# Kernel optimization log

Hardware: AMD Instinct MI355X
Metric: run time of the kernel (lower is better)

## Reference

```python
import jax, jax.numpy as jnp
import numpy as np
import math

N, S, D, BF, K, NT, NL = 4096, 64, 256, 24, 8, 64, 4096

def setup_inputs() -> dict:
    key = jax.random.key(0)
    ks = jax.random.split(key, 20)
    inp = {
        "values": jax.random.normal(ks[0], (N, S), dtype=jnp.float32),
        "kinds": jax.random.randint(ks[1], (N, S), 0, K, dtype=jnp.int32),
        "mask": jax.random.randint(ks[2], (N, S), 0, 2, dtype=jnp.int32),
        "prim_type": jax.random.randint(ks[3], (N,), 0, NT, dtype=jnp.int32),
        "layer_id": jax.random.randint(ks[4], (N,), 0, NL, dtype=jnp.int32),
        "meta": jax.random.normal(ks[5], (N, 4), dtype=jnp.float32),
        # frozen Fourier projection (sigma=8)
        "B_ff": jax.random.normal(ks[6], (1, BF), dtype=jnp.float32) * 8.0,
        # embeddings (N(0,1) like nn.Embedding default)
        "kind_emb_w": jax.random.normal(ks[7], (K, D), dtype=jnp.float32),
        "type_emb_w": jax.random.normal(ks[8], (NT, D), dtype=jnp.float32),
        "layer_emb_w": jax.random.normal(ks[9], (NL, D), dtype=jnp.float32),
        # per-kind MLPs: 2B -> D -> D
        "mlp_w1": jax.random.normal(ks[10], (K, 2 * BF, D), dtype=jnp.float32) / np.sqrt(2 * BF),
        "mlp_b1": jnp.zeros((K, D), dtype=jnp.float32),
        "mlp_w2": jax.random.normal(ks[11], (K, D, D), dtype=jnp.float32) / np.sqrt(D),
        "mlp_b2": jnp.zeros((K, D), dtype=jnp.float32),
        # fuse: 3D -> D -> D
        "fuse_w1": jax.random.normal(ks[12], (3 * D, D), dtype=jnp.float32) / np.sqrt(3 * D),
        "fuse_b1": jnp.zeros((D,), dtype=jnp.float32),
        "fuse_w2": jax.random.normal(ks[13], (D, D), dtype=jnp.float32) / np.sqrt(D),
        "fuse_b2": jnp.zeros((D,), dtype=jnp.float32),
        # meta_lin: 4 -> D
        "meta_w": jax.random.normal(ks[14], (4, D), dtype=jnp.float32) / 2.0,
        "meta_b": jnp.zeros((D,), dtype=jnp.float32),
    }
    return inp

def _gelu(x):
    return jax.nn.gelu(x, approximate=False)  # torch nn.GELU default = exact erf

def reference(values, kinds, mask, prim_type, layer_id, meta, B_ff,
              kind_emb_w, type_emb_w, layer_emb_w,
              mlp_w1, mlp_b1, mlp_w2, mlp_b2,
              fuse_w1, fuse_b1, fuse_w2, fuse_b2, meta_w, meta_b):
    n, s = values.shape
    d = kind_emb_w.shape[1]
    k_kinds = kind_emb_w.shape[0]
    # Fourier features over all N*S scalar slots -> [NS, 2B]
    y = (2.0 * math.pi) * values.reshape(-1, 1) @ B_ff
    ff = jnp.concatenate([jnp.sin(y), jnp.cos(y)], axis=-1)
    kf = kinds.reshape(-1)
    # kind-routed per-kind MLP (dispatch/combine expressed as masked combine)
    out = jnp.zeros((n * s, d), dtype=values.dtype)
    for k in range(k_kinds):
        h = _gelu(ff @ mlp_w1[k] + mlp_b1[k]) @ mlp_w2[k] + mlp_b2[k]
        out = jnp.where((kf == k)[:, None], h, out)
    h_slots = out.reshape(n, s, d) + kind_emb_w[kinds]
    m = mask.astype(values.dtype)
    h_slots = h_slots * m[..., None]
    denom = jnp.clip(m.sum(axis=1, keepdims=True), 1.0)  # [N,1]
    h_num = h_slots.sum(axis=1) / denom  # masked mean pooling -> [N,D]
    h = jnp.concatenate([h_num, type_emb_w[prim_type], layer_emb_w[layer_id]], axis=-1)
    fused = _gelu(h @ fuse_w1 + fuse_b1) @ fuse_w2 + fuse_b2
    return fused + meta @ meta_w + meta_b
```

## Files before the change

kernel.cpp:

```cpp
#include <hip/hip_runtime.h>
#include <math.h>


#define W2F_HI   0
#define W2F_LO   524288
#define W1F_HI   1048576
#define W1F_LO   1179648
#define FW1F_HI  1310720
#define FW1F_LO  1507328
#define FW2F_HI  1703936
#define FW2F_LO  1769472

#define PSTR 260

typedef __attribute__((ext_vector_type(8))) short frag;
typedef __attribute__((ext_vector_type(4))) float f32x4;

__device__ __forceinline__ unsigned short f2bf_rn(float x) {
    unsigned int u = __float_as_uint(x);
    unsigned int r = (u + 0x7fffu + ((u >> 16) & 1u)) >> 16;
    return (unsigned short)r;
}
__device__ __forceinline__ float bf2f(unsigned short h) {
    return __uint_as_float(((unsigned int)h) << 16);
}
__device__ __forceinline__ void split_bf(float x, unsigned short& h, unsigned short& l) {
    unsigned short hh = f2bf_rn(x);
    h = hh;
    l = f2bf_rn(x - bf2f(hh));
}

__device__ __forceinline__ float gelu_fast(float x) {
    float u = fabsf(x) * 0.7071067811865476f;
    float t = __builtin_amdgcn_rcpf(fmaf(0.3275911f, u, 1.0f));
    float p = fmaf(fmaf(fmaf(fmaf(1.061405429f, t, -1.453152027f), t,
                             1.421413741f), t, -0.284496736f), t, 0.254829592f) * t;
    float e = __expf(-u * u);
    float er = fmaf(-p, e, 1.0f);
    er = copysignf(er, x);
    return 0.5f * x * (1.0f + er);
}

__global__ __launch_bounds__(512) void prep_kernel(
    const float* __restrict__ w1, const float* __restrict__ w2,
    const float* __restrict__ fw1, const float* __restrict__ fw2,
    short* __restrict__ ws)
{
    int tid = blockIdx.x * 512 + threadIdx.x;
    int fid = tid >> 6, ln = tid & 63;
    if (fid >= 1792) return;
    int lr = ln & 15, kq = ln >> 4;
    float v[8];
    int dhi, dlo, dsto;
    if (fid < 1024) {
        int k = fid >> 7, kst = (fid >> 4) & 7, nt = fid & 15;
        int col = nt * 16 + lr;
        #pragma unroll
        for (int b = 0; b < 8; ++b) {
            int kg = kst * 32 + kq * 8 + b;
            v[b] = w2[(k * 256 + kg) * 256 + col];
        }
        dsto = fid * 512 + ln * 8; dhi = W2F_HI; dlo = W2F_LO;
    } else if (fid < 1280) {
        int f = fid - 1024;
        int k = f >> 5, kst = (f >> 4) & 1, nt = f & 15;
        int col = nt * 16 + lr;
        #pragma unroll
        for (int b = 0; b < 8; ++b) {
            int kg = kst * 32 + kq * 8 + b;
            v[b] = (kg < 48) ? w1[(k * 48 + kg) * 256 + col] : 0.0f;
        }
        dsto = f * 512 + ln * 8; dhi = W1F_HI; dlo = W1F_LO;
    } else if (fid < 1664) {
        int f = fid - 1280;
        int kst = f >> 4, nt = f & 15;
        int col = nt * 16 + lr;
        #pragma unroll
        for (int b = 0; b < 8; ++b) {
            int kg = kst * 32 + kq * 8 + b;
            v[b] = fw1[kg * 256 + col];
        }
        dsto = f * 512 + ln * 8; dhi = FW1F_HI; dlo = FW1F_LO;
    } else {
        int f = fid - 1664;
        int kst = f >> 4, nt = f & 15;
        int col = nt * 16 + lr;
        #pragma unroll
        for (int b = 0; b < 8; ++b) {
            int kg = kst * 32 + kq * 8 + b;
            v[b] = fw2[kg * 256 + col];
        }
        dsto = f * 512 + ln * 8; dhi = FW2F_HI; dlo = FW2F_LO;
    }
    union { unsigned short u[8]; frag f; } hu, lu;
    #pragma unroll
    for (int b = 0; b < 8; ++b) split_bf(v[b], hu.u[b], lu.u[b]);
    *(frag*)(ws + dhi + dsto) = hu.f;
    *(frag*)(ws + dlo + dsto) = lu.f;
}

__global__ __launch_bounds__(512, 1) void mono_kernel(
    const float* __restrict__ values, const int* __restrict__ kinds,
    const int* __restrict__ mask, const float* __restrict__ B_ff,
    const float* __restrict__ b1, const short* __restrict__ wsf,
    const int* __restrict__ pt, const int* __restrict__ lid,
    const float* __restrict__ meta, const float* __restrict__ type_emb,
    const float* __restrict__ layer_emb, const float* __restrict__ b2,
    const float* __restrict__ kind_emb, const float* __restrict__ fb1,
    const float* __restrict__ fb2, const float* __restrict__ meta_w,
    const float* __restrict__ meta_b, float* __restrict__ out)
{
    __shared__ __align__(16) float pool_ls[8 * 16 * PSTR];
    __shared__ float vals_ls[1024];
    __shared__ unsigned char knd_ls[1024], msk_ls[1024];
    __shared__ unsigned short list[1152];
    __shared__ short chunk_kind[80], chunk_base[80];
    __shared__ int totk_ls[8];
    __shared__ float b1_ls[2048];
    __shared__ float Bs_ls[24];
    __shared__ float cnt_ls[128], den_ls[16], meta_ls[64];
    __shared__ int pt_ls[16], lid_ls[16];

    const int t = threadIdx.x, blk = blockIdx.x;
    const int wv = t >> 6, ln = t & 63, lr16 = ln & 15, kq = ln >> 4;
    const int gbase = blk * 1024, rb = blk * 16;

    const short* w1f_hi  = wsf + W1F_HI;
    const short* w1f_lo  = wsf + W1F_LO;
    const short* w2f_hi  = wsf + W2F_HI;
    const short* w2f_lo  = wsf + W2F_LO;
    const short* fw1f_hi = wsf + FW1F_HI;
    const short* fw1f_lo = wsf + FW1F_LO;
    const short* fw2f_hi = wsf + FW2F_HI;
    const short* fw2f_lo = wsf + FW2F_LO;

    #pragma unroll
    for (int i = 0; i < 2; ++i) {
        int p = t + i * 512;
        vals_ls[p] = values[gbase + p];
        knd_ls[p]  = (unsigned char)kinds[gbase + p];
        msk_ls[p]  = (unsigned char)mask[gbase + p];
    }
    #pragma unroll
    for (int i = 0; i < 4; ++i) b1_ls[t + i * 512] = b1[t + i * 512];
    if (t < 24) Bs_ls[t] = B_ff[t];
    if (t >= 32 && t < 48) { pt_ls[t - 32] = pt[rb + t - 32]; lid_ls[t - 32] = lid[rb + t - 32]; }
    if (t >= 64 && t < 128) meta_ls[t - 64] = meta[rb * 4 + (t - 64)];
    for (int i = t; i < 8 * 16 * PSTR; i += 512) pool_ls[i] = 0.0f;
    __syncthreads();

    {
        const int k = wv;
        int tot = 0;
        #pragma unroll 1
        for (int c = 0; c < 16; ++c) {
            int p = c * 64 + ln;
            int kd = knd_ls[p], mk = msk_ls[p];
            unsigned long long bal = __ballot(mk && (kd == k));
            int pc = __popcll(bal);
            if (ln == 0) cnt_ls[c * 8 + k] = (float)pc;
            tot += pc;
            if (k == 0) {
                unsigned long long balm = __ballot(mk != 0);
                if (ln == 0) {
                    int tm = __popcll(balm);
                    den_ls[c] = 1.0f / (float)(tm > 0 ? tm : 1);
                }
            }
        }
        if (ln == 0) totk_ls[k] = tot;
    }
    __syncthreads();

    int offe = 0, cbase = 0, nch = 0;
    #pragma unroll
    for (int j = 0; j < 8; ++j) {
        int pj = (totk_ls[j] + 15) & ~15;
        if (j < wv) { offe += pj; cbase += pj >> 4; }
        nch += pj >> 4;
    }

    {
        const int k = wv;
        const unsigned long long below = (1ull << ln) - 1ull;
        int fill = 0;
        #pragma unroll 1
        for (int c = 0; c < 16; ++c) {
            int p = c * 64 + ln;
            int kd = knd_ls[p], mk = msk_ls[p];
            unsigned long long bal = __ballot(mk && (kd == k));
            if (mk && (kd == k)) list[offe + fill + __popcll(bal & below)] = (unsigned short)p;
            fill += __popcll(bal);
        }
        int padded = (fill + 15) & ~15;
        for (int i = fill + ln; i < padded; i += 64) list[offe + i] = 0xFFFFu;
        int nk = padded >> 4;
        for (int j = ln; j < nk; j += 64) {
            chunk_kind[cbase + j] = (short)k;
            chunk_base[cbase + j] = (short)(offe + j * 16);
        }
    }
    __syncthreads();

    for (int m = wv; m < nch; m += 8) {
        const int k = (int)chunk_kind[m];
        const int cb = (int)chunk_base[m];
        int slot = list[cb + lr16];
        float v = vals_ls[slot & 1023];
        v = (slot == 0xFFFF) ? 0.0f : v;

        frag ah[2], al[2];
        #pragma unroll
        for (int kst = 0; kst < 2; ++kst) {
            union { unsigned short u[8]; frag f; } hu, lu;
            int jb0 = kst * 32 + kq * 8;
            #pragma unroll
            for (int b = 0; b < 8; ++b) {
                int jb = jb0 + b;
                float sv;
                if (jb < 48) {
                    int jm = (jb < 24) ? jb : jb - 24;
                    float cadd = (jb < 24) ? 0.0f : 0.25f;
                    float rev = __builtin_amdgcn_fractf(fmaf(v, Bs_ls[jm], cadd));
                    sv = __builtin_amdgcn_sinf(rev);
                } else {
                    sv = 0.0f;
                }
                split_bf(sv, hu.u[b], lu.u[b]);
            }
            ah[kst] = hu.f; al[kst] = lu.f;
        }

        int e4[4];
        #pragma unroll
        for (int r = 0; r < 4; ++r) {
            int sl = list[cb + kq * 4 + r];
            e4[r] = (sl == 0xFFFF) ? -1 : ((sl >> 6) & 15);
        }

        #pragma unroll 4
        for (int nt = 0; nt < 16; ++nt) {
            int o0 = ((k * 2 + 0) * 16 + nt) * 512 + ln * 8;
            int o1 = ((k * 2 + 1) * 16 + nt) * 512 + ln * 8;
            frag bh0 = *(const frag*)(w1f_hi + o0);
            frag bl0 = *(const frag*)(w1f_lo + o0);
            frag bh1 = *(const frag*)(w1f_hi + o1);
            frag bl1 = *(const frag*)(w1f_lo + o1);
            f32x4 acc = (f32x4)0.0f;
            acc = __builtin_amdgcn_mfma_f32_16x16x32_bf16(ah[0], bh0, acc, 0, 0, 0);
            acc = __builtin_amdgcn_mfma_f32_16x16x32_bf16(al[0], bh0, acc, 0, 0, 0);
            acc = __builtin_amdgcn_mfma_f32_16x16x32_bf16(ah[0], bl0, acc, 0, 0, 0);
            acc = __builtin_amdgcn_mfma_f32_16x16x32_bf16(ah[1], bh1, acc, 0, 0, 0);
            acc = __builtin_amdgcn_mfma_f32_16x16x32_bf16(al[1], bh1, acc, 0, 0, 0);
            acc = __builtin_amdgcn_mfma_f32_16x16x32_bf16(ah[1], bl1, acc, 0, 0, 0);
            float b1v = b1_ls[k * 256 + nt * 16 + lr16];
            #pragma unroll
            for (int r = 0; r < 4; ++r) {
                if (e4[r] >= 0) {
                    float g = gelu_fast(acc[r] + b1v);
                    atomicAdd(&pool_ls[(k * 16 + e4[r]) * PSTR + nt * 16 + lr16], g);
                }
            }
        }
    }
    __syncthreads();

    f32x4 acc[2];
    acc[0] = (f32x4)0.0f; acc[1] = (f32x4)0.0f;

    for (int k = 0; k < 8; ++k) {
        #pragma unroll 2
        for (int kst = 0; kst < 8; ++kst) {
            const float* pp = &pool_ls[(k * 16 + lr16) * PSTR + kst * 32 + kq * 8];
            f32x4 u0 = *(const f32x4*)pp;
            f32x4 u1 = *(const f32x4*)(pp + 4);
            union { unsigned short u[8]; frag f; } hu, lu;
            #pragma unroll
            for (int b = 0; b < 4; ++b) {
                split_bf(u0[b], hu.u[b], lu.u[b]);
                split_bf(u1[b], hu.u[b + 4], lu.u[b + 4]);
            }
            frag ah = hu.f, al = lu.f;
            #pragma unroll
            for (int n = 0; n < 2; ++n) {
                int bo = ((k * 8 + kst) * 16 + (wv * 2 + n)) * 512 + ln * 8;
                frag bh = *(const frag*)(w2f_hi + bo);
                frag bl = *(const frag*)(w2f_lo + bo);
                acc[n] = __builtin_amdgcn_mfma_f32_16x16x32_bf16(ah, bh, acc[n], 0, 0, 0);
                acc[n] = __builtin_amdgcn_mfma_f32_16x16x32_bf16(al, bh, acc[n], 0, 0, 0);
                acc[n] = __builtin_amdgcn_mfma_f32_16x16x32_bf16(ah, bl, acc[n], 0, 0, 0);
            }
        }
    }
    __syncthreads();

    float* hz = pool_ls;

    #pragma unroll
    for (int n = 0; n < 2; ++n) {
        int col = (wv * 2 + n) * 16 + lr16;
        float bks[8];
        #pragma unroll
        for (int k = 0; k < 8; ++k) bks[k] = b2[k * 256 + col] + kind_emb[k * 256 + col];
        #pragma unroll
        for (int r = 0; r < 4; ++r) {
            int row = kq * 4 + r;
            float hv = acc[n][r];
            #pragma unroll
            for (int k = 0; k < 8; ++k) hv = fmaf(cnt_ls[row * 8 + k], bks[k], hv);
            hv *= den_ls[row];
            hz[row * 256 + ((((col >> 2) ^ (row & 7)) << 2) | (col & 3))] = hv;
        }
    }
    __syncthreads();

    f32x4 az[2];
    az[0] = (f32x4)0.0f; az[1] = (f32x4)0.0f;

    for (int kst = 0; kst < 24; ++kst) {
        const int row = lr16;
        union { unsigned short u[8]; frag f; } hu, lu;
        if (kst < 8) {
            int c0 = kst * 8 + kq * 2;
            f32x4 u0 = *(const f32x4*)&hz[row * 256 + ((c0 ^ (row & 7)) << 2)];
            f32x4 u1 = *(const f32x4*)&hz[row * 256 + (((c0 + 1) ^ (row & 7)) << 2)];
            #pragma unroll
            for (int b = 0; b < 4; ++b) {
                split_bf(u0[b], hu.u[b], lu.u[b]);
                split_bf(u1[b], hu.u[b + 4], lu.u[b + 4]);
            }
        } else {
            const float* eb = (kst < 16) ? type_emb : layer_emb;
            const int* ids = (kst < 16) ? pt_ls : lid_ls;
            int ko = (kst & 7) * 32 + kq * 8;
            const float* sp = eb + (size_t)ids[row] * 256 + ko;
            f32x4 u0 = *(const f32x4*)sp;
            f32x4 u1 = *(const f32x4*)(sp + 4);
            #pragma unroll
            for (int b = 0; b < 4; ++b) {
                split_bf(u0[b], hu.u[b], lu.u[b]);
                split_bf(u1[b], hu.u[b + 4], lu.u[b + 4]);
            }
        }
        frag ah = hu.f, al = lu.f;
        #pragma unroll
        for (int n = 0; n < 2; ++n) {
            int bo = (kst * 16 + (wv * 2 + n)) * 512 + ln * 8;
            frag bh = *(const frag*)(fw1f_hi + bo);
            frag bl = *(const frag*)(fw1f_lo + bo);
            az[n] = __builtin_amdgcn_mfma_f32_16x16x32_bf16(ah, bh, az[n], 0, 0, 0);
            az[n] = __builtin_amdgcn_mfma_f32_16x16x32_bf16(al, bh, az[n], 0, 0, 0);
            az[n] = __builtin_amdgcn_mfma_f32_16x16x32_bf16(ah, bl, az[n], 0, 0, 0);
        }
    }
    __syncthreads();

    #pragma unroll
    for (int n = 0; n < 2; ++n) {
        int col = (wv * 2 + n) * 16 + lr16;
        float fb1v = fb1[col];
        #pragma unroll
        for (int r = 0; r < 4; ++r) {
            int row = kq * 4 + r;
            float z = gelu_fast(az[n][r] + fb1v);
            hz[row * 256 + ((((col >> 2) ^ (row & 7)) << 2) | (col & 3))] = z;
        }
    }
    __syncthreads();

    f32x4 ao2[2];
    ao2[0] = (f32x4)0.0f; ao2[1] = (f32x4)0.0f;

    for (int kst = 0; kst < 8; ++kst) {
        const int row = lr16;
        int c0 = kst * 8 + kq * 2;
        f32x4 u0 = *(const f32x4*)&hz[row * 256 + ((c0 ^ (row & 7)) << 2)];
        f32x4 u1 = *(const f32x4*)&hz[row * 256 + (((c0 + 1) ^ (row & 7)) << 2)];
        union { unsigned short u[8]; frag f; } hu, lu;
        #pragma unroll
        for (int b = 0; b < 4; ++b) {
            split_bf(u0[b], hu.u[b], lu.u[b]);
            split_bf(u1[b], hu.u[b + 4], lu.u[b + 4]);
        }
        frag ah = hu.f, al = lu.f;
        #pragma unroll
        for (int n = 0; n < 2; ++n) {
            int bo = (kst * 16 + (wv * 2 + n)) * 512 + ln * 8;
            frag bh = *(const frag*)(fw2f_hi + bo);
            frag bl = *(const frag*)(fw2f_lo + bo);
            ao2[n] = __builtin_amdgcn_mfma_f32_16x16x32_bf16(ah, bh, ao2[n], 0, 0, 0);
            ao2[n] = __builtin_amdgcn_mfma_f32_16x16x32_bf16(al, bh, ao2[n], 0, 0, 0);
            ao2[n] = __builtin_amdgcn_mfma_f32_16x16x32_bf16(ah, bl, ao2[n], 0, 0, 0);
        }
    }

    #pragma unroll
    for (int n = 0; n < 2; ++n) {
        int col = (wv * 2 + n) * 16 + lr16;
        float ob = fb2[col] + meta_b[col];
        float mw0 = meta_w[col], mw1 = meta_w[256 + col];
        float mw2 = meta_w[512 + col], mw3 = meta_w[768 + col];
        #pragma unroll
        for (int r = 0; r < 4; ++r) {
            int row = kq * 4 + r;
            float o = ao2[n][r] + ob;
            o = fmaf(meta_ls[row * 4 + 0], mw0, o);
            o = fmaf(meta_ls[row * 4 + 1], mw1, o);
            o = fmaf(meta_ls[row * 4 + 2], mw2, o);
            o = fmaf(meta_ls[row * 4 + 3], mw3, o);
            out[(size_t)(rb + row) * 256 + col] = o;
        }
    }
}

extern "C" void kernel_launch(void* const* d_in, const int* in_sizes, int n_in,
                              void* d_out, int out_size, void* d_ws, size_t ws_size,
                              hipStream_t stream) {
    const float* values    = (const float*)d_in[0];
    const int*   kinds     = (const int*)d_in[1];
    const int*   mask      = (const int*)d_in[2];
    const int*   prim_type = (const int*)d_in[3];
    const int*   layer_id  = (const int*)d_in[4];
    const float* meta      = (const float*)d_in[5];
    const float* B_ff      = (const float*)d_in[6];
    const float* kind_emb  = (const float*)d_in[7];
    const float* type_emb  = (const float*)d_in[8];
    const float* layer_emb = (const float*)d_in[9];
    const float* mlp_w1    = (const float*)d_in[10];
    const float* mlp_b1    = (const float*)d_in[11];
    const float* mlp_w2    = (const float*)d_in[12];
    const float* mlp_b2    = (const float*)d_in[13];
    const float* fuse_w1   = (const float*)d_in[14];
    const float* fuse_b1   = (const float*)d_in[15];
    const float* fuse_w2   = (const float*)d_in[16];
    const float* fuse_b2   = (const float*)d_in[17];
    const float* meta_w    = (const float*)d_in[18];
    const float* meta_b    = (const float*)d_in[19];

    short* ws  = (short*)d_ws;
    float* out = (float*)d_out;

    prep_kernel<<<224, 512, 0, stream>>>(mlp_w1, mlp_w2, fuse_w1, fuse_w2, ws);
    mono_kernel<<<256, 512, 0, stream>>>(values, kinds, mask, B_ff, mlp_b1, ws,
                                         prim_type, layer_id, meta, type_emb,
                                         layer_emb, mlp_b2, kind_emb, fuse_b1,
                                         fuse_b2, meta_w, meta_b, out);
}
```

Baseline: 248.7 us.

## Halve rows per block to launch 512 blocks with smaller LDS footprint

Each block now handles 8 rows (512 slots) instead of 16, which doubles the grid to 512 blocks and halves the pooling buffer and slot-list shared memory. Launch bounds now allow several blocks per CU, so all 256 CUs get work and latency can be hidden across blocks. The fuse-stage MFMAs still use 16-row tiles, so half of each tile is duplicated or padding work. Per-block fixed costs such as loading b1 and the MLP weights are also repeated across twice as many blocks.

```diff
diff --git a/kernel.cpp b/kernel.cpp
--- a/kernel.cpp
+++ b/kernel.cpp
@@ -12,6 +12,8 @@
 #define FW2F_LO  1769472
 
 #define PSTR 260
+#define WIN  512
+#define ROWS 8
 
 typedef __attribute__((ext_vector_type(8))) short frag;
 typedef __attribute__((ext_vector_type(4))) float f32x4;
@@ -99,7 +101,7 @@
     *(frag*)(ws + dlo + dsto) = lu.f;
 }
 
-__global__ __launch_bounds__(512, 1) void mono_kernel(
+__global__ __launch_bounds__(512, 4) void mono_kernel(
     const float* __restrict__ values, const int* __restrict__ kinds,
     const int* __restrict__ mask, const float* __restrict__ B_ff,
     const float* __restrict__ b1, const short* __restrict__ wsf,
@@ -110,20 +112,20 @@
     const float* __restrict__ fb2, const float* __restrict__ meta_w,
     const float* __restrict__ meta_b, float* __restrict__ out)
 {
-    __shared__ __align__(16) float pool_ls[8 * 16 * PSTR];
-    __shared__ float vals_ls[1024];
-    __shared__ unsigned char knd_ls[1024], msk_ls[1024];
-    __shared__ unsigned short list[1152];
-    __shared__ short chunk_kind[80], chunk_base[80];
+    __shared__ __align__(16) float pool_ls[8 * ROWS * PSTR];
+    __shared__ float vals_ls[WIN];
+    __shared__ unsigned char knd_ls[WIN], msk_ls[WIN];
+    __shared__ unsigned short list[640];
+    __shared__ short chunk_kind[48], chunk_base[48];
     __shared__ int totk_ls[8];
     __shared__ float b1_ls[2048];
     __shared__ float Bs_ls[24];
-    __shared__ float cnt_ls[128], den_ls[16], meta_ls[64];
-    __shared__ int pt_ls[16], lid_ls[16];
+    __shared__ float cnt_ls[ROWS * 8], den_ls[ROWS], meta_ls[ROWS * 4];
+    __shared__ int pt_ls[ROWS], lid_ls[ROWS];
 
     const int t = threadIdx.x, blk = blockIdx.x;
     const int wv = t >> 6, ln = t & 63, lr16 = ln & 15, kq = ln >> 4;
-    const int gbase = blk * 1024, rb = blk * 16;
+    const int gbase = blk * WIN, rb = blk * ROWS;
 
     const short* w1f_hi  = wsf + W1F_HI;
     const short* w1f_lo  = wsf + W1F_LO;
@@ -134,26 +136,24 @@
     const short* fw2f_hi = wsf + FW2F_HI;
     const short* fw2f_lo = wsf + FW2F_LO;
 
-    #pragma unroll
-    for (int i = 0; i < 2; ++i) {
-        int p = t + i * 512;
-        vals_ls[p] = values[gbase + p];
-        knd_ls[p]  = (unsigned char)kinds[gbase + p];
-        msk_ls[p]  = (unsigned char)mask[gbase + p];
+    {
+        vals_ls[t] = values[gbase + t];
+        knd_ls[t]  = (unsigned char)kinds[gbase + t];
+        msk_ls[t]  = (unsigned char)mask[gbase + t];
     }
     #pragma unroll
     for (int i = 0; i < 4; ++i) b1_ls[t + i * 512] = b1[t + i * 512];
     if (t < 24) Bs_ls[t] = B_ff[t];
-    if (t >= 32 && t < 48) { pt_ls[t - 32] = pt[rb + t - 32]; lid_ls[t - 32] = lid[rb + t - 32]; }
-    if (t >= 64 && t < 128) meta_ls[t - 64] = meta[rb * 4 + (t - 64)];
-    for (int i = t; i < 8 * 16 * PSTR; i += 512) pool_ls[i] = 0.0f;
+    if (t >= 32 && t < 32 + ROWS) { pt_ls[t - 32] = pt[rb + t - 32]; lid_ls[t - 32] = lid[rb + t - 32]; }
+    if (t >= 64 && t < 64 + ROWS * 4) meta_ls[t - 64] = meta[rb * 4 + (t - 64)];
+    for (int i = t; i < 8 * ROWS * PSTR; i += 512) pool_ls[i] = 0.0f;
     __syncthreads();
 
     {
         const int k = wv;
         int tot = 0;
         #pragma unroll 1
-        for (int c = 0; c < 16; ++c) {
+        for (int c = 0; c < ROWS; ++c) {
             int p = c * 64 + ln;
             int kd = knd_ls[p], mk = msk_ls[p];
             unsigned long long bal = __ballot(mk && (kd == k));
@@ -185,7 +185,7 @@
         const unsigned long long below = (1ull << ln) - 1ull;
         int fill = 0;
         #pragma unroll 1
-        for (int c = 0; c < 16; ++c) {
+        for (int c = 0; c < ROWS; ++c) {
             int p = c * 64 + ln;
             int kd = knd_ls[p], mk = msk_ls[p];
             unsigned long long bal = __ballot(mk && (kd == k));
@@ -206,7 +206,7 @@
         const int k = (int)chunk_kind[m];
         const int cb = (int)chunk_base[m];
         int slot = list[cb + lr16];
-        float v = vals_ls[slot & 1023];
+        float v = vals_ls[slot & (WIN - 1)];
         v = (slot == 0xFFFF) ? 0.0f : v;
 
         frag ah[2], al[2];
@@ -235,7 +235,7 @@
         #pragma unroll
         for (int r = 0; r < 4; ++r) {
             int sl = list[cb + kq * 4 + r];
-            e4[r] = (sl == 0xFFFF) ? -1 : ((sl >> 6) & 15);
+            e4[r] = (sl == 0xFFFF) ? -1 : ((sl >> 6) & 7);
         }
 
         #pragma unroll 4
@@ -258,7 +258,7 @@
             for (int r = 0; r < 4; ++r) {
                 if (e4[r] >= 0) {
                     float g = gelu_fast(acc[r] + b1v);
-                    atomicAdd(&pool_ls[(k * 16 + e4[r]) * PSTR + nt * 16 + lr16], g);
+                    atomicAdd(&pool_ls[(k * ROWS + e4[r]) * PSTR + nt * 16 + lr16], g);
                 }
             }
         }
@@ -271,7 +271,7 @@
     for (int k = 0; k < 8; ++k) {
         #pragma unroll 2
         for (int kst = 0; kst < 8; ++kst) {
-            const float* pp = &pool_ls[(k * 16 + lr16) * PSTR + kst * 32 + kq * 8];
+            const float* pp = &pool_ls[(k * ROWS + (lr16 & 7)) * PSTR + kst * 32 + kq * 8];
             f32x4 u0 = *(const f32x4*)pp;
             f32x4 u1 = *(const f32x4*)(pp + 4);
             union { unsigned short u[8]; frag f; } hu, lu;
@@ -296,20 +296,22 @@
 
     float* hz = pool_ls;
 
-    #pragma unroll
-    for (int n = 0; n < 2; ++n) {
-        int col = (wv * 2 + n) * 16 + lr16;
-        float bks[8];
-        #pragma unroll
-        for (int k = 0; k < 8; ++k) bks[k] = b2[k * 256 + col] + kind_emb[k * 256 + col];
-        #pragma unroll
-        for (int r = 0; r < 4; ++r) {
-            int row = kq * 4 + r;
-            float hv = acc[n][r];
-            #pragma unroll
-            for (int k = 0; k < 8; ++k) hv = fmaf(cnt_ls[row * 8 + k], bks[k], hv);
-            hv *= den_ls[row];
-            hz[row * 256 + ((((col >> 2) ^ (row & 7)) << 2) | (col & 3))] = hv;
+    if (kq < 2) {
+        #pragma unroll
+        for (int n = 0; n < 2; ++n) {
+            int col = (wv * 2 + n) * 16 + lr16;
+            float bks[8];
+            #pragma unroll
+            for (int k = 0; k < 8; ++k) bks[k] = b2[k * 256 + col] + kind_emb[k * 256 + col];
+            #pragma unroll
+            for (int r = 0; r < 4; ++r) {
+                int row = kq * 4 + r;
+                float hv = acc[n][r];
+                #pragma unroll
+                for (int k = 0; k < 8; ++k) hv = fmaf(cnt_ls[row * 8 + k], bks[k], hv);
+                hv *= den_ls[row];
+                hz[row * 256 + ((((col >> 2) ^ (row & 7)) << 2) | (col & 3))] = hv;
+            }
         }
     }
     __syncthreads();
@@ -318,12 +320,12 @@
     az[0] = (f32x4)0.0f; az[1] = (f32x4)0.0f;
 
     for (int kst = 0; kst < 24; ++kst) {
-        const int row = lr16;
+        const int row = lr16 & 7;
         union { unsigned short u[8]; frag f; } hu, lu;
         if (kst < 8) {
             int c0 = kst * 8 + kq * 2;
-            f32x4 u0 = *(const f32x4*)&hz[row * 256 + ((c0 ^ (row & 7)) << 2)];
-            f32x4 u1 = *(const f32x4*)&hz[row * 256 + (((c0 + 1) ^ (row & 7)) << 2)];
+            f32x4 u0 = *(const f32x4*)&hz[row * 256 + ((c0 ^ row) << 2)];
+            f32x4 u1 = *(const f32x4*)&hz[row * 256 + (((c0 + 1) ^ row) << 2)];
             #pragma unroll
             for (int b = 0; b < 4; ++b) {
                 split_bf(u0[b], hu.u[b], lu.u[b]);
@@ -355,15 +357,17 @@
     }
     __syncthreads();
 
-    #pragma unroll
-    for (int n = 0; n < 2; ++n) {
-        int col = (wv * 2 + n) * 16 + lr16;
-        float fb1v = fb1[col];
-        #pragma unroll
-        for (int r = 0; r < 4; ++r) {
-            int row = kq * 4 + r;
-            float z = gelu_fast(az[n][r] + fb1v);
-            hz[row * 256 + ((((col >> 2) ^ (row & 7)) << 2) | (col & 3))] = z;
+    if (kq < 2) {
+        #pragma unroll
+        for (int n = 0; n < 2; ++n) {
+            int col = (wv * 2 + n) * 16 + lr16;
+            float fb1v = fb1[col];
+            #pragma unroll
+            for (int r = 0; r < 4; ++r) {
+                int row = kq * 4 + r;
+                float z = gelu_fast(az[n][r] + fb1v);
+                hz[row * 256 + ((((col >> 2) ^ row) << 2) | (col & 3))] = z;
+            }
         }
     }
     __syncthreads();
@@ -372,10 +376,10 @@
     ao2[0] = (f32x4)0.0f; ao2[1] = (f32x4)0.0f;
 
     for (int kst = 0; kst < 8; ++kst) {
-        const int row = lr16;
+        const int row = lr16 & 7;
         int c0 = kst * 8 + kq * 2;
-        f32x4 u0 = *(const f32x4*)&hz[row * 256 + ((c0 ^ (row & 7)) << 2)];
-        f32x4 u1 = *(const f32x4*)&hz[row * 256 + (((c0 + 1) ^ (row & 7)) << 2)];
+        f32x4 u0 = *(const f32x4*)&hz[row * 256 + ((c0 ^ row) << 2)];
+        f32x4 u1 = *(const f32x4*)&hz[row * 256 + (((c0 + 1) ^ row) << 2)];
         union { unsigned short u[8]; frag f; } hu, lu;
         #pragma unroll
         for (int b = 0; b < 4; ++b) {
@@ -394,21 +398,23 @@
         }
     }
 
-    #pragma unroll
-    for (int n = 0; n < 2; ++n) {
-        int col = (wv * 2 + n) * 16 + lr16;
-        float ob = fb2[col] + meta_b[col];
-        float mw0 = meta_w[col], mw1 = meta_w[256 + col];
-        float mw2 = meta_w[512 + col], mw3 = meta_w[768 + col];
-        #pragma unroll
-        for (int r = 0; r < 4; ++r) {
-            int row = kq * 4 + r;
-            float o = ao2[n][r] + ob;
-            o = fmaf(meta_ls[row * 4 + 0], mw0, o);
-            o = fmaf(meta_ls[row * 4 + 1], mw1, o);
-            o = fmaf(meta_ls[row * 4 + 2], mw2, o);
-            o = fmaf(meta_ls[row * 4 + 3], mw3, o);
-            out[(size_t)(rb + row) * 256 + col] = o;
+    if (kq < 2) {
+        #pragma unroll
+        for (int n = 0; n < 2; ++n) {
+            int col = (wv * 2 + n) * 16 + lr16;
+            float ob = fb2[col] + meta_b[col];
+            float mw0 = meta_w[col], mw1 = meta_w[256 + col];
+            float mw2 = meta_w[512 + col], mw3 = meta_w[768 + col];
+            #pragma unroll
+            for (int r = 0; r < 4; ++r) {
+                int row = kq * 4 + r;
+                float o = ao2[n][r] + ob;
+                o = fmaf(meta_ls[row * 4 + 0], mw0, o);
+                o = fmaf(meta_ls[row * 4 + 1], mw1, o);
+                o = fmaf(meta_ls[row * 4 + 2], mw2, o);
+                o = fmaf(meta_ls[row * 4 + 3], mw3, o);
+                out[(size_t)(rb + row) * 256 + col] = o;
+            }
         }
     }
 }
@@ -441,7 +447,7 @@
     float* out = (float*)d_out;
 
     prep_kernel<<<224, 512, 0, stream>>>(mlp_w1, mlp_w2, fuse_w1, fuse_w2, ws);
-    mono_kernel<<<256, 512, 0, stream>>>(values, kinds, mask, B_ff, mlp_b1, ws,
+    mono_kernel<<<512, 512, 0, stream>>>(values, kinds, mask, B_ff, mlp_b1, ws,
                                          prim_type, layer_id, meta, type_emb,
                                          layer_emb, mlp_b2, kind_emb, fuse_b1,
                                          fuse_b2, meta_w, meta_b, out);
```

New measurement: 266.0 us. +7.0%, slower.
